# Optimization experiments

Measured on AMD Instinct MI355X. Metric: run time of the kernel, lower is better.

The kernel has to match this reference:

```python
import jax, jax.numpy as jnp
import numpy as np

B, L, IN_DIM, OUT_DIM = 8, 128, 512, 512
DEP_NUM, DEP_DIM = 45, 16


def setup_inputs() -> dict:
    key = jax.random.key(0)
    ks = jax.random.split(key, 10)
    h = jax.random.normal(ks[0], (B, L, IN_DIM), dtype=jnp.float32)
    dep_type_matrix = jax.random.randint(ks[1], (B, L, L), 0, DEP_NUM, dtype=jnp.int32)
    aspect_mask = jnp.zeros((B, L), dtype=bool).at[:, 10:14].set(True)
    # params (torch Linear convention: y = x @ W.T + b); xavier-ish scale
    def xavier(k, shape):
        fan_in, fan_out = shape[1], shape[0]
        lim = jnp.sqrt(6.0 / (fan_in + fan_out))
        return jax.random.uniform(k, shape, jnp.float32, -lim, lim)
    emb = jax.random.normal(ks[2], (DEP_NUM, DEP_DIM), dtype=jnp.float32)
    W1 = xavier(ks[3], (OUT_DIM, IN_DIM + DEP_DIM))
    b1 = jnp.zeros((OUT_DIM,), jnp.float32)
    W2 = xavier(ks[4], (OUT_DIM, IN_DIM + DEP_DIM))
    b2 = jnp.zeros((OUT_DIM,), jnp.float32)
    Wg = xavier(ks[5], (OUT_DIM, IN_DIM))
    bg = jnp.zeros((OUT_DIM,), jnp.float32)
    bias = jnp.zeros((OUT_DIM,), jnp.float32)
    return {"h": h, "dep_type_matrix": dep_type_matrix, "aspect_mask": aspect_mask,
            "emb": emb, "W1": W1, "b1": b1, "W2": W2, "b2": b2,
            "Wg": Wg, "bg": bg, "bias": bias}


def _position_aware(h, aspect_mask):
    # h: [B,L,D], aspect_mask: [B,L] bool
    Lh = h.shape[1]
    m = aspect_mask.astype(jnp.int32)
    start = jnp.argmax(m, axis=1)                       # first True
    end = Lh - 1 - jnp.argmax(jnp.flip(m, axis=1), axis=1)  # last True
    pos = jnp.arange(Lh)[None, :]                        # [1,L]
    s = start[:, None]
    e = end[:, None]
    inv_L = 1.0 / Lh
    left_w = 1.0 - (s - pos).astype(h.dtype) * inv_L
    right_w = 1.0 - (pos - e).astype(h.dtype) * inv_L
    w = jnp.where(pos < s, left_w, jnp.where(pos > e, right_w, 0.0))
    w = jnp.where(aspect_mask, 0.0, w)                   # zero on aspect words
    return h * w[:, :, None]


def reference(h, dep_type_matrix, aspect_mask, emb, W1, b1, W2, b2, Wg, bg, bias):
    D = h.shape[-1]
    h = _position_aware(h, aspect_mask)
    dep_emb = emb[dep_type_matrix]                       # [B,L,L,E]
    # split concat-linear: W(concat[h_i, e_ij]) = h_i @ Wh.T + e_ij @ Wd.T + b
    W1h, W1d = W1[:, :D], W1[:, D:]
    W2h, W2d = W2[:, :D], W2[:, D:]
    hp_i = jnp.einsum('bid,od->bio', h, W1h)[:, :, None, :] \
        + jnp.einsum('bije,oe->bijo', dep_emb, W1d) + b1   # [B,L,L,O]
    hp_j = jnp.einsum('bid,od->bio', h, W2h)[:, :, None, :] \
        + jnp.einsum('bije,oe->bijo', dep_emb, W2d) + b2   # [B,L,L,O]
    scores = jnp.exp(jnp.sum(hp_i * hp_j, axis=-1))        # [B,L,L]
    adj = (dep_type_matrix != 0).astype(scores.dtype)
    masked = scores * adj
    A = masked / (jnp.sum(masked, axis=-1, keepdims=True) + 1e-6)
    h_trans = jnp.einsum('bid,od->bio', h, Wg) + bg        # [B,L,O]
    out = jnp.einsum('bij,bjo->bio', A, h_trans) + bias
    return jax.nn.relu(out)
```

## Files before the change

kernel.cpp:

```cpp
#include <hip/hip_runtime.h>
#include <hip/hip_bf16.h>
#include <math.h>

#define NBATCH 8
#define NL 128
#define IND 512
#define DEPN 45
#define DEPD 16
#define WCOLS 528
#define NP 1664
#define C_P1 0
#define C_P2 512
#define C_HT 1024
#define C_D1 1536
#define C_D2 1581
#define C_PAD 1626

typedef __attribute__((ext_vector_type(8))) short bf16x8;
typedef __attribute__((ext_vector_type(4))) float f32x4;

__device__ inline ushort f2bf(float x) {
    __hip_bfloat16 b = __float2bfloat16(x);
    return *reinterpret_cast<ushort*>(&b);
}
__device__ inline float bf2f(ushort u) {
    __hip_bfloat16 b;
    *reinterpret_cast<ushort*>(&b) = u;
    return __bfloat162float(b);
}

__device__ __forceinline__ void gl16(const ushort* g, ushort* l) {
    __builtin_amdgcn_global_load_lds(
        (const __attribute__((address_space(1))) unsigned int*)g,
        (__attribute__((address_space(3))) unsigned int*)l, 16, 0, 0);
}

__global__ __launch_bounds__(256) void k_prep(
    const float* __restrict__ h, const unsigned char* __restrict__ mask,
    const float* __restrict__ emb,
    const float* __restrict__ W1, const float* __restrict__ W2,
    const float* __restrict__ Wg,
    const float* __restrict__ b1, const float* __restrict__ b2,
    const float* __restrict__ bg,
    ushort* __restrict__ A_hi, ushort* __restrict__ A_lo,
    ushort* __restrict__ B_hi, ushort* __restrict__ B_lo,
    float* __restrict__ bias_ext) {
    int bid = blockIdx.x;
    int tid = threadIdx.x;

    if (bid < 64) {
        int rb = bid * 16;
        int b = rb >> 7;
        __shared__ int sflag, smin, smax;
        __shared__ float w16[16];
        if (tid == 0) { sflag = 0; smin = NL; smax = -1; }
        __syncthreads();
        const int* mi = (const int*)mask;
        if (tid < 128) {
            int v0 = mi[tid], v1 = mi[tid + 128];
            if ((unsigned)v0 > 1u || (unsigned)v1 > 1u) atomicOr(&sflag, 1);
        }
        __syncthreads();
        if (tid < 128) {
            int mval = sflag ? (int)mask[b * NL + tid] : mi[b * NL + tid];
            if (mval) { atomicMin(&smin, tid); atomicMax(&smax, tid); }
        }
        __syncthreads();
        if (tid < 16) {
            int any = (smax >= 0);
            int s = any ? smin : 0;
            int e = any ? smax : (NL - 1);
            int i = (rb & 127) + tid;
            const float invL = 1.0f / (float)NL;
            float w;
            if (i < s)      w = 1.0f - (float)(s - i) * invL;
            else if (i > e) w = 1.0f - (float)(i - e) * invL;
            else            w = 0.0f;
            int mval = sflag ? (int)mask[b * NL + i] : mi[b * NL + i];
            if (mval) w = 0.0f;
            w16[tid] = w;
        }
        __syncthreads();
        for (int idx = tid; idx < 16 * 128; idx += 256) {
            int r = idx >> 7, dc = (idx & 127) << 2;
            float4 hv = *(const float4*)&h[(size_t)(rb + r) * IND + dc];
            float wv = w16[r];
            hv.x *= wv; hv.y *= wv; hv.z *= wv; hv.w *= wv;
            ushort4 hi4, lo4;
            hi4.x = f2bf(hv.x); hi4.y = f2bf(hv.y); hi4.z = f2bf(hv.z); hi4.w = f2bf(hv.w);
            lo4.x = f2bf(hv.x - bf2f(hi4.x));
            lo4.y = f2bf(hv.y - bf2f(hi4.y));
            lo4.z = f2bf(hv.z - bf2f(hi4.z));
            lo4.w = f2bf(hv.w - bf2f(hi4.w));
            *(ushort4*)&A_hi[(size_t)(rb + r) * IND + dc] = hi4;
            *(ushort4*)&A_lo[(size_t)(rb + r) * IND + dc] = lo4;
        }
        if (bid == 0) {
            for (int i = tid; i < 512; i += 256) {
                bias_ext[C_P1 + i] = b1[i];
                bias_ext[C_P2 + i] = b2[i];
                bias_ext[C_HT + i] = bg[i];
            }
            if (tid < NP - C_PAD) bias_ext[C_PAD + tid] = 0.f;
        }
    } else if (bid < 160) {
        int nb = (bid - 64) * 16;
        for (int idx = tid; idx < 16 * 128; idx += 256) {
            int r = idx >> 7, dc = (idx & 127) << 2;
            int n = nb + r;
            const float* src;
            if (n < 512)       src = W1 + (size_t)n * WCOLS + dc;
            else if (n < 1024) src = W2 + (size_t)(n - 512) * WCOLS + dc;
            else               src = Wg + (size_t)(n - 1024) * IND + dc;
            float4 wv = *(const float4*)src;
            ushort4 hi4;
            hi4.x = f2bf(wv.x); hi4.y = f2bf(wv.y); hi4.z = f2bf(wv.z); hi4.w = f2bf(wv.w);
            *(ushort4*)&B_hi[(size_t)n * IND + dc] = hi4;
            if (n >= 1024) {
                ushort4 lo4;
                lo4.x = f2bf(wv.x - bf2f(hi4.x));
                lo4.y = f2bf(wv.y - bf2f(hi4.y));
                lo4.z = f2bf(wv.z - bf2f(hi4.z));
                lo4.w = f2bf(wv.w - bf2f(hi4.w));
                *(ushort4*)&B_lo[(size_t)n * IND + dc] = lo4;
            }
        }
    } else if (bid < 162) {
        int nb = 1626 + (bid - 160) * 19;
        ushort4 z4 = {0, 0, 0, 0};
        for (int idx = tid; idx < 19 * 128; idx += 256) {
            int r = idx >> 7, dc = (idx & 127) << 2;
            *(ushort4*)&B_hi[(size_t)(nb + r) * IND + dc] = z4;
            *(ushort4*)&B_lo[(size_t)(nb + r) * IND + dc] = z4;
        }
    } else if (bid < 234) {
        int zi = bid - 162;
        int m = zi / 36;
        int rest = zi % 36;
        int dq = rest / 9;
        int tq = rest % 9;
        int tb = tq * 5;
        __shared__ float es5[5][DEPD];
        __shared__ float ys5[5][512];
        __shared__ float part[5][256];
        if (tid < 5 * DEPD) es5[tid >> 4][tid & 15] = emb[(tb + (tid >> 4)) * DEPD + (tid & 15)];
        __syncthreads();
        const float* Wdep = (m == 0) ? W2 : W1;
        for (int idx = tid; idx < 5 * 512; idx += 256) {
            int tt = idx >> 9, o = idx & 511;
            float s = 0.f;
#pragma unroll
            for (int e = 0; e < DEPD; e++) s += es5[tt][e] * Wdep[o * WCOLS + IND + e];
            ys5[tt][o] = s;
        }
        __syncthreads();
        int dloc = tid & 127, half = tid >> 7;
        const float* Wsrc = (m == 0) ? W1 : W2;
        int d = dq * 128 + dloc;
        int obase = half * 256;
        float ac0 = 0.f, ac1 = 0.f, ac2 = 0.f, ac3 = 0.f, ac4 = 0.f;
#pragma unroll 8
        for (int oo = 0; oo < 256; oo++) {
            float w = Wsrc[(size_t)(obase + oo) * WCOLS + d];
            int o = obase + oo;
            ac0 += w * ys5[0][o];
            ac1 += w * ys5[1][o];
            ac2 += w * ys5[2][o];
            ac3 += w * ys5[3][o];
            ac4 += w * ys5[4][o];
        }
        part[0][tid] = ac0; part[1][tid] = ac1; part[2][tid] = ac2;
        part[3][tid] = ac3; part[4][tid] = ac4;
        __syncthreads();
        if (half == 0) {
#pragma unroll
            for (int tt = 0; tt < 5; tt++) {
                float tot = part[tt][dloc] + part[tt][128 + dloc];
                int row = ((m == 0) ? C_D1 : C_D2) + tb + tt;
                ushort hi = f2bf(tot);
                B_hi[(size_t)row * IND + d] = hi;
                B_lo[(size_t)row * IND + d] = f2bf(tot - bf2f(hi));
            }
        }
    } else {
        int zi2 = bid - 234;
        int t = zi2 % 45;
        int m = zi2 / 45;
        __shared__ float es[DEPD];
        __shared__ float ys[512];
        __shared__ float y1s[512];
        if (tid < DEPD) es[tid] = emb[t * DEPD + tid];
        __syncthreads();
        const float* Wdep = (m == 0) ? W2 : W1;
        for (int o = tid; o < 512; o += 256) {
            float s = 0.f;
#pragma unroll
            for (int e = 0; e < DEPD; e++) s += es[e] * Wdep[o * WCOLS + IND + e];
            ys[o] = s;
        }
        if (m == 0) {
            for (int o = tid; o < 512; o += 256) {
                float s = 0.f;
#pragma unroll
                for (int e = 0; e < DEPD; e++) s += es[e] * W1[o * WCOLS + IND + e];
                y1s[o] = s;
            }
        }
        __syncthreads();
        if (tid < 64) {
            const float* bb = (m == 0) ? b1 : b2;
            float sb = 0.f;
#pragma unroll
            for (int k = 0; k < 8; k++) sb += bb[tid + k * 64] * ys[tid + k * 64];
            if (m == 0) {
#pragma unroll
                for (int k = 0; k < 8; k++) sb += y1s[tid + k * 64] * ys[tid + k * 64];
            }
            for (int off = 32; off; off >>= 1) sb += __shfl_down(sb, off, 64);
            if (tid == 0) bias_ext[((m == 0) ? C_D1 : C_D2) + t] = sb;
        }
    }
}

__global__ __launch_bounds__(256) void k3_gemm(
    const ushort* __restrict__ A_hi, const ushort* __restrict__ A_lo,
    const ushort* __restrict__ B_hi, const ushort* __restrict__ B_lo,
    const float* __restrict__ bias_ext, float* __restrict__ Pout,
    ushort* __restrict__ HTb) {
    int tid = threadIdx.x;
    int wid = tid >> 6, lane = tid & 63;
    int lrow = lane & 15;
    int mbase = blockIdx.x * 64;
    int nbase = blockIdx.y * 64;
    int mh = (wid >> 1) << 5;
    int nh = (wid & 1) << 5;

    __shared__ ushort Ah[2][8 * 64 * 8];
    __shared__ ushort Al[2][8 * 64 * 8];
    __shared__ ushort Bh[2][8 * 64 * 8];
    __shared__ ushort Bl[2][8 * 64 * 8];

    const ushort* aH = A_hi + (size_t)(mbase + lane) * IND;
    const ushort* aL = A_lo + (size_t)(mbase + lane) * IND;
    const ushort* bH = B_hi + (size_t)(nbase + lane) * IND;
    const ushort* bL = B_lo + (size_t)(nbase + lane) * IND;

    f32x4 acc00 = {0.f, 0.f, 0.f, 0.f};
    f32x4 acc01 = acc00, acc10 = acc00, acc11 = acc00;

    if (nbase >= C_HT) {
#define STAGE(BUF, C) { \
    int ck = (C) << 6; \
    if (wid == 0) { \
        _Pragma("unroll") \
        for (int g = 0; g < 8; g++) gl16(aH + ck + (g << 3), &Ah[BUF][g << 9]); \
    } else if (wid == 1) { \
        _Pragma("unroll") \
        for (int g = 0; g < 8; g++) gl16(aL + ck + (g << 3), &Al[BUF][g << 9]); \
    } else if (wid == 2) { \
        _Pragma("unroll") \
        for (int g = 0; g < 8; g++) gl16(bH + ck + (g << 3), &Bh[BUF][g << 9]); \
    } else { \
        _Pragma("unroll") \
        for (int g = 0; g < 8; g++) gl16(bL + ck + (g << 3), &Bl[BUF][g << 9]); \
    } }
        STAGE(0, 0)
        for (int c = 0; c < 8; c++) {
            int cb = c & 1;
            __syncthreads();
            if (c < 7) STAGE(cb ^ 1, c + 1)
#pragma unroll
            for (int KS = 0; KS < 2; KS++) {
                int gA = (KS << 2) + (lane >> 4);
                int ga = ((gA << 6) + mh + lrow) << 3;
                int gb = ((gA << 6) + nh + lrow) << 3;
                bf16x8 a0h = *(const bf16x8*)&Ah[cb][ga];
                bf16x8 a0l = *(const bf16x8*)&Al[cb][ga];
                bf16x8 a1h = *(const bf16x8*)&Ah[cb][ga + 128];
                bf16x8 a1l = *(const bf16x8*)&Al[cb][ga + 128];
                bf16x8 b0h = *(const bf16x8*)&Bh[cb][gb];
                bf16x8 b0l = *(const bf16x8*)&Bl[cb][gb];
                bf16x8 b1h = *(const bf16x8*)&Bh[cb][gb + 128];
                bf16x8 b1l = *(const bf16x8*)&Bl[cb][gb + 128];
                acc00 = __builtin_amdgcn_mfma_f32_16x16x32_bf16(a0h, b0h, acc00, 0, 0, 0);
                acc00 = __builtin_amdgcn_mfma_f32_16x16x32_bf16(a0h, b0l, acc00, 0, 0, 0);
                acc00 = __builtin_amdgcn_mfma_f32_16x16x32_bf16(a0l, b0h, acc00, 0, 0, 0);
                acc01 = __builtin_amdgcn_mfma_f32_16x16x32_bf16(a0h, b1h, acc01, 0, 0, 0);
                acc01 = __builtin_amdgcn_mfma_f32_16x16x32_bf16(a0h, b1l, acc01, 0, 0, 0);
                acc01 = __builtin_amdgcn_mfma_f32_16x16x32_bf16(a0l, b1h, acc01, 0, 0, 0);
                acc10 = __builtin_amdgcn_mfma_f32_16x16x32_bf16(a1h, b0h, acc10, 0, 0, 0);
                acc10 = __builtin_amdgcn_mfma_f32_16x16x32_bf16(a1h, b0l, acc10, 0, 0, 0);
                acc10 = __builtin_amdgcn_mfma_f32_16x16x32_bf16(a1l, b0h, acc10, 0, 0, 0);
                acc11 = __builtin_amdgcn_mfma_f32_16x16x32_bf16(a1h, b1h, acc11, 0, 0, 0);
                acc11 = __builtin_amdgcn_mfma_f32_16x16x32_bf16(a1h, b1l, acc11, 0, 0, 0);
                acc11 = __builtin_amdgcn_mfma_f32_16x16x32_bf16(a1l, b1h, acc11, 0, 0, 0);
            }
        }
#undef STAGE
    } else {
#define STAGEL(BUF, C) { \
    int ck = (C) << 6; \
    if (wid == 0) { \
        _Pragma("unroll") \
        for (int g = 0; g < 4; g++) gl16(aH + ck + (g << 3), &Ah[BUF][g << 9]); \
    } else if (wid == 1) { \
        _Pragma("unroll") \
        for (int g = 4; g < 8; g++) gl16(aH + ck + (g << 3), &Ah[BUF][g << 9]); \
    } else if (wid == 2) { \
        _Pragma("unroll") \
        for (int g = 0; g < 4; g++) gl16(bH + ck + (g << 3), &Bh[BUF][g << 9]); \
    } else { \
        _Pragma("unroll") \
        for (int g = 4; g < 8; g++) gl16(bH + ck + (g << 3), &Bh[BUF][g << 9]); \
    } }
        STAGEL(0, 0)
        for (int c = 0; c < 8; c++) {
            int cb = c & 1;
            __syncthreads();
            if (c < 7) STAGEL(cb ^ 1, c + 1)
#pragma unroll
            for (int KS = 0; KS < 2; KS++) {
                int gA = (KS << 2) + (lane >> 4);
                int ga = ((gA << 6) + mh + lrow) << 3;
                int gb = ((gA << 6) + nh + lrow) << 3;
                bf16x8 a0h = *(const bf16x8*)&Ah[cb][ga];
                bf16x8 a1h = *(const bf16x8*)&Ah[cb][ga + 128];
                bf16x8 b0h = *(const bf16x8*)&Bh[cb][gb];
                bf16x8 b1h = *(const bf16x8*)&Bh[cb][gb + 128];
                acc00 = __builtin_amdgcn_mfma_f32_16x16x32_bf16(a0h, b0h, acc00, 0, 0, 0);
                acc01 = __builtin_amdgcn_mfma_f32_16x16x32_bf16(a0h, b1h, acc01, 0, 0, 0);
                acc10 = __builtin_amdgcn_mfma_f32_16x16x32_bf16(a1h, b0h, acc10, 0, 0, 0);
                acc11 = __builtin_amdgcn_mfma_f32_16x16x32_bf16(a1h, b1h, acc11, 0, 0, 0);
            }
        }
#undef STAGEL
    }

    int r0 = (lane >> 4) << 2;
    int colb = nbase + nh;
    int col0 = colb + lrow;
    int col1 = col0 + 16;
    float bv0 = bias_ext[col0];
    float bv1 = bias_ext[col1];
    int rowb = mbase + mh;

    if (colb >= C_HT && colb < C_HT + 512) {
        int o0 = col0 - C_HT, o1 = col1 - C_HT;
#pragma unroll
        for (int r = 0; r < 4; ++r) {
            int row0 = rowb + r0 + r;
            int row1 = row0 + 16;
            HTb[(size_t)row0 * 512 + o0] = f2bf(acc00[r] + bv0);
            HTb[(size_t)row0 * 512 + o1] = f2bf(acc01[r] + bv1);
            HTb[(size_t)row1 * 512 + o0] = f2bf(acc10[r] + bv0);
            HTb[(size_t)row1 * 512 + o1] = f2bf(acc11[r] + bv1);
        }
    } else {
#pragma unroll
        for (int r = 0; r < 4; ++r) {
            int row0 = rowb + r0 + r;
            int row1 = row0 + 16;
            Pout[(size_t)row0 * NP + col0] = acc00[r] + bv0;
            Pout[(size_t)row0 * NP + col1] = acc01[r] + bv1;
            Pout[(size_t)row1 * NP + col0] = acc10[r] + bv0;
            Pout[(size_t)row1 * NP + col1] = acc11[r] + bv1;
        }
    }
}

__global__ __launch_bounds__(256) void k5_out(
    const float* __restrict__ P, const int* __restrict__ dep,
    const ushort* __restrict__ HTb, const float* __restrict__ bias,
    float* __restrict__ out) {
    int blk = blockIdx.x;
    int b = blk >> 5;
    int i0 = b * 128 + (blk & 31) * 4;
    int tid = threadIdx.x;
    int wr = tid >> 6, lane = tid & 63;
    __shared__ float a[4][NL];
    __shared__ float c0s[4];
    __shared__ float comb[4][48];
    __shared__ float invs[4];

    {
        const float* p1 = P + (size_t)(i0 + wr) * NP + C_P1 + lane * 8;
        const float* p2 = P + (size_t)(i0 + wr) * NP + C_P2 + lane * 8;
        float4 x0 = *(const float4*)(p1);
        float4 x1 = *(const float4*)(p1 + 4);
        float4 y0 = *(const float4*)(p2);
        float4 y1 = *(const float4*)(p2 + 4);
        float s = x0.x * y0.x + x0.y * y0.y + x0.z * y0.z + x0.w * y0.w
                + x1.x * y1.x + x1.y * y1.y + x1.z * y1.z + x1.w * y1.w;
        for (int off = 32; off; off >>= 1) s += __shfl_down(s, off, 64);
        if (lane == 0) c0s[wr] = s;
    }
    for (int idx = tid; idx < 4 * 45; idx += 256) {
        int r = idx / 45, t = idx - r * 45;
        const float* Prow = P + (size_t)(i0 + r) * NP;
        comb[r][t] = Prow[C_D1 + t] + Prow[C_D2 + t];
    }
    __syncthreads();

#pragma unroll
    for (int k = 0; k < 2; k++) {
        int idx = tid + k * 256;
        int r = idx >> 7, j = idx & 127;
        int tt = dep[(size_t)(i0 + r) * NL + j];
        a[r][j] = (tt != 0) ? expf(c0s[r] + comb[r][tt]) : 0.f;
    }
    __syncthreads();
    {
        float v = a[wr][lane] + a[wr][lane + 64];
        for (int off = 32; off; off >>= 1) v += __shfl_down(v, off, 64);
        if (lane == 0) invs[wr] = 1.0f / (v + 1e-6f);
    }
    __syncthreads();

    int o2 = tid * 2;
    float s00 = 0.f, s01 = 0.f, s10 = 0.f, s11 = 0.f;
    float s20 = 0.f, s21 = 0.f, s30 = 0.f, s31 = 0.f;
    const ushort* hp = HTb + (size_t)b * NL * 512 + o2;
#pragma unroll 8
    for (int j = 0; j < NL; j++) {
        ushort2 hv = *(const ushort2*)(hp + (size_t)j * 512);
        float h0 = bf2f(hv.x), h1 = bf2f(hv.y);
        float a0 = a[0][j], a1 = a[1][j], a2 = a[2][j], a3 = a[3][j];
        s00 += a0 * h0; s01 += a0 * h1;
        s10 += a1 * h0; s11 += a1 * h1;
        s20 += a2 * h0; s21 += a2 * h1;
        s30 += a3 * h0; s31 += a3 * h1;
    }
    float bv0 = bias[o2], bv1 = bias[o2 + 1];
    float i0v = invs[0], i1v = invs[1], i2v = invs[2], i3v = invs[3];
    float2 o;
    o.x = fmaxf(s00 * i0v + bv0, 0.f); o.y = fmaxf(s01 * i0v + bv1, 0.f);
    *(float2*)&out[(size_t)(i0 + 0) * 512 + o2] = o;
    o.x = fmaxf(s10 * i1v + bv0, 0.f); o.y = fmaxf(s11 * i1v + bv1, 0.f);
    *(float2*)&out[(size_t)(i0 + 1) * 512 + o2] = o;
    o.x = fmaxf(s20 * i2v + bv0, 0.f); o.y = fmaxf(s21 * i2v + bv1, 0.f);
    *(float2*)&out[(size_t)(i0 + 2) * 512 + o2] = o;
    o.x = fmaxf(s30 * i3v + bv0, 0.f); o.y = fmaxf(s31 * i3v + bv1, 0.f);
    *(float2*)&out[(size_t)(i0 + 3) * 512 + o2] = o;
}

extern "C" void kernel_launch(void* const* d_in, const int* in_sizes, int n_in,
                              void* d_out, int out_size, void* d_ws, size_t ws_size,
                              hipStream_t stream) {
    const float* h    = (const float*)d_in[0];
    const int* dep    = (const int*)d_in[1];
    const unsigned char* mask = (const unsigned char*)d_in[2];
    const float* emb  = (const float*)d_in[3];
    const float* W1   = (const float*)d_in[4];
    const float* b1   = (const float*)d_in[5];
    const float* W2   = (const float*)d_in[6];
    const float* b2   = (const float*)d_in[7];
    const float* Wg   = (const float*)d_in[8];
    const float* bg   = (const float*)d_in[9];
    const float* bias = (const float*)d_in[10];
    float* out = (float*)d_out;

    char* p = (char*)d_ws;
    ushort* A_hi = (ushort*)p;  p += (size_t)1024 * 512 * 2;
    ushort* A_lo = (ushort*)p;  p += (size_t)1024 * 512 * 2;
    ushort* B_hi = (ushort*)p;  p += (size_t)NP * 512 * 2;
    ushort* B_lo = (ushort*)p;  p += (size_t)NP * 512 * 2;
    ushort* HTb = (ushort*)p;   p += (size_t)1024 * 512 * 2;
    float* bias_ext = (float*)p; p += NP * 4;
    float* Pout = (float*)p;

    k_prep<<<324, 256, 0, stream>>>(h, mask, emb, W1, W2, Wg, b1, b2, bg,
                                    A_hi, A_lo, B_hi, B_lo, bias_ext);
    dim3 g3(16, 26);
    k3_gemm<<<g3, 256, 0, stream>>>(A_hi, A_lo, B_hi, B_lo, bias_ext, Pout, HTb);
    k5_out<<<256, 256, 0, stream>>>(Pout, dep, HTb, bias, out);
}
```

Baseline: 48.32 us.

## Fuse P1·P2 row dot product into GEMM epilogue with atomic accumulation

The GEMM blocks for the two projection column ranges now compute both the W1h and W2h tiles together against the same A tile, so the A tile is loaded once for both. Each block forms the partial per-row dot product of the biased projections in registers, reduces it with shuffles, and atomically adds it into a new c0 buffer. This removes the full 512-column fp32 P1/P2 writes and the matching reads in the output kernel, and shrinks the grid from 26 to 18 column blocks. In exchange it adds atomics, which make the summation order nondeterministic, and it needs a zero-init of the buffer in the prep kernel.

```diff
diff --git a/kernel.cpp b/kernel.cpp
--- a/kernel.cpp
+++ b/kernel.cpp
@@ -44,7 +44,7 @@
     const float* __restrict__ bg,
     ushort* __restrict__ A_hi, ushort* __restrict__ A_lo,
     ushort* __restrict__ B_hi, ushort* __restrict__ B_lo,
-    float* __restrict__ bias_ext) {
+    float* __restrict__ bias_ext, float* __restrict__ c0buf) {
     int bid = blockIdx.x;
     int tid = threadIdx.x;
 
@@ -102,6 +102,7 @@
                 bias_ext[C_HT + i] = bg[i];
             }
             if (tid < NP - C_PAD) bias_ext[C_PAD + tid] = 0.f;
+            for (int i = tid; i < 1024; i += 256) c0buf[i] = 0.f;
         }
     } else if (bid < 160) {
         int nb = (bid - 64) * 16;
@@ -226,29 +227,30 @@
     const ushort* __restrict__ A_hi, const ushort* __restrict__ A_lo,
     const ushort* __restrict__ B_hi, const ushort* __restrict__ B_lo,
     const float* __restrict__ bias_ext, float* __restrict__ Pout,
-    ushort* __restrict__ HTb) {
+    ushort* __restrict__ HTb, float* __restrict__ c0buf) {
     int tid = threadIdx.x;
     int wid = tid >> 6, lane = tid & 63;
     int lrow = lane & 15;
     int mbase = blockIdx.x * 64;
-    int nbase = blockIdx.y * 64;
+    int y = blockIdx.y;
     int mh = (wid >> 1) << 5;
     int nh = (wid & 1) << 5;
+    int r0 = (lane >> 4) << 2;
+    int rowb = mbase + mh;
 
     __shared__ ushort Ah[2][8 * 64 * 8];
     __shared__ ushort Al[2][8 * 64 * 8];
     __shared__ ushort Bh[2][8 * 64 * 8];
     __shared__ ushort Bl[2][8 * 64 * 8];
 
-    const ushort* aH = A_hi + (size_t)(mbase + lane) * IND;
-    const ushort* aL = A_lo + (size_t)(mbase + lane) * IND;
-    const ushort* bH = B_hi + (size_t)(nbase + lane) * IND;
-    const ushort* bL = B_lo + (size_t)(nbase + lane) * IND;
-
-    f32x4 acc00 = {0.f, 0.f, 0.f, 0.f};
-    f32x4 acc01 = acc00, acc10 = acc00, acc11 = acc00;
-
-    if (nbase >= C_HT) {
+    if (y >= 8) {
+        int nbase = 1024 + ((y - 8) << 6);
+        const ushort* aH = A_hi + (size_t)(mbase + lane) * IND;
+        const ushort* aL = A_lo + (size_t)(mbase + lane) * IND;
+        const ushort* bH = B_hi + (size_t)(nbase + lane) * IND;
+        const ushort* bL = B_lo + (size_t)(nbase + lane) * IND;
+        f32x4 acc00 = {0.f, 0.f, 0.f, 0.f};
+        f32x4 acc01 = acc00, acc10 = acc00, acc11 = acc00;
 #define STAGE(BUF, C) { \
     int ck = (C) << 6; \
     if (wid == 0) { \
@@ -297,27 +299,58 @@
             }
         }
 #undef STAGE
+        int colb = nbase + nh;
+        int col0 = colb + lrow;
+        int col1 = col0 + 16;
+        float bv0 = bias_ext[col0];
+        float bv1 = bias_ext[col1];
+        if (colb < C_D1) {
+            int o0 = col0 - C_HT, o1 = col1 - C_HT;
+#pragma unroll
+            for (int r = 0; r < 4; ++r) {
+                int row0 = rowb + r0 + r;
+                int row1 = row0 + 16;
+                HTb[(size_t)row0 * 512 + o0] = f2bf(acc00[r] + bv0);
+                HTb[(size_t)row0 * 512 + o1] = f2bf(acc01[r] + bv1);
+                HTb[(size_t)row1 * 512 + o0] = f2bf(acc10[r] + bv0);
+                HTb[(size_t)row1 * 512 + o1] = f2bf(acc11[r] + bv1);
+            }
+        } else {
+#pragma unroll
+            for (int r = 0; r < 4; ++r) {
+                int row0 = rowb + r0 + r;
+                int row1 = row0 + 16;
+                Pout[(size_t)row0 * NP + col0] = acc00[r] + bv0;
+                Pout[(size_t)row0 * NP + col1] = acc01[r] + bv1;
+                Pout[(size_t)row1 * NP + col0] = acc10[r] + bv0;
+                Pout[(size_t)row1 * NP + col1] = acc11[r] + bv1;
+            }
+        }
     } else {
-#define STAGEL(BUF, C) { \
+        int j = y;
+        const ushort* aH  = A_hi + (size_t)(mbase + lane) * IND;
+        const ushort* b1H = B_hi + (size_t)((j << 6) + lane) * IND;
+        const ushort* b2H = B_hi + (size_t)(512 + (j << 6) + lane) * IND;
+        f32x4 z4 = {0.f, 0.f, 0.f, 0.f};
+        f32x4 p00 = z4, p01 = z4, p10 = z4, p11 = z4;
+        f32x4 q00 = z4, q01 = z4, q10 = z4, q11 = z4;
+#define STAGEP(BUF, C) { \
     int ck = (C) << 6; \
     if (wid == 0) { \
         _Pragma("unroll") \
-        for (int g = 0; g < 4; g++) gl16(aH + ck + (g << 3), &Ah[BUF][g << 9]); \
+        for (int g = 0; g < 8; g++) gl16(aH + ck + (g << 3), &Ah[BUF][g << 9]); \
     } else if (wid == 1) { \
         _Pragma("unroll") \
-        for (int g = 4; g < 8; g++) gl16(aH + ck + (g << 3), &Ah[BUF][g << 9]); \
+        for (int g = 0; g < 8; g++) gl16(b1H + ck + (g << 3), &Bh[BUF][g << 9]); \
     } else if (wid == 2) { \
         _Pragma("unroll") \
-        for (int g = 0; g < 4; g++) gl16(bH + ck + (g << 3), &Bh[BUF][g << 9]); \
-    } else { \
-        _Pragma("unroll") \
-        for (int g = 4; g < 8; g++) gl16(bH + ck + (g << 3), &Bh[BUF][g << 9]); \
+        for (int g = 0; g < 8; g++) gl16(b2H + ck + (g << 3), &Al[BUF][g << 9]); \
     } }
-        STAGEL(0, 0)
+        STAGEP(0, 0)
         for (int c = 0; c < 8; c++) {
             int cb = c & 1;
             __syncthreads();
-            if (c < 7) STAGEL(cb ^ 1, c + 1)
+            if (c < 7) STAGEP(cb ^ 1, c + 1)
 #pragma unroll
             for (int KS = 0; KS < 2; KS++) {
                 int gA = (KS << 2) + (lane >> 4);
@@ -325,45 +358,38 @@
                 int gb = ((gA << 6) + nh + lrow) << 3;
                 bf16x8 a0h = *(const bf16x8*)&Ah[cb][ga];
                 bf16x8 a1h = *(const bf16x8*)&Ah[cb][ga + 128];
-                bf16x8 b0h = *(const bf16x8*)&Bh[cb][gb];
-                bf16x8 b1h = *(const bf16x8*)&Bh[cb][gb + 128];
-                acc00 = __builtin_amdgcn_mfma_f32_16x16x32_bf16(a0h, b0h, acc00, 0, 0, 0);
-                acc01 = __builtin_amdgcn_mfma_f32_16x16x32_bf16(a0h, b1h, acc01, 0, 0, 0);
-                acc10 = __builtin_amdgcn_mfma_f32_16x16x32_bf16(a1h, b0h, acc10, 0, 0, 0);
-                acc11 = __builtin_amdgcn_mfma_f32_16x16x32_bf16(a1h, b1h, acc11, 0, 0, 0);
-            }
-        }
-#undef STAGEL
-    }
-
-    int r0 = (lane >> 4) << 2;
-    int colb = nbase + nh;
-    int col0 = colb + lrow;
-    int col1 = col0 + 16;
-    float bv0 = bias_ext[col0];
-    float bv1 = bias_ext[col1];
-    int rowb = mbase + mh;
-
-    if (colb >= C_HT && colb < C_HT + 512) {
-        int o0 = col0 - C_HT, o1 = col1 - C_HT;
+                bf16x8 b10 = *(const bf16x8*)&Bh[cb][gb];
+                bf16x8 b11 = *(const bf16x8*)&Bh[cb][gb + 128];
+                bf16x8 b20 = *(const bf16x8*)&Al[cb][gb];
+                bf16x8 b21 = *(const bf16x8*)&Al[cb][gb + 128];
+                p00 = __builtin_amdgcn_mfma_f32_16x16x32_bf16(a0h, b10, p00, 0, 0, 0);
+                p01 = __builtin_amdgcn_mfma_f32_16x16x32_bf16(a0h, b11, p01, 0, 0, 0);
+                p10 = __builtin_amdgcn_mfma_f32_16x16x32_bf16(a1h, b10, p10, 0, 0, 0);
+                p11 = __builtin_amdgcn_mfma_f32_16x16x32_bf16(a1h, b11, p11, 0, 0, 0);
+                q00 = __builtin_amdgcn_mfma_f32_16x16x32_bf16(a0h, b20, q00, 0, 0, 0);
+                q01 = __builtin_amdgcn_mfma_f32_16x16x32_bf16(a0h, b21, q01, 0, 0, 0);
+                q10 = __builtin_amdgcn_mfma_f32_16x16x32_bf16(a1h, b20, q10, 0, 0, 0);
+                q11 = __builtin_amdgcn_mfma_f32_16x16x32_bf16(a1h, b21, q11, 0, 0, 0);
+            }
+        }
+#undef STAGEP
+        int o0 = (j << 6) + nh + lrow;
+        float b1v0 = bias_ext[C_P1 + o0], b1v1 = bias_ext[C_P1 + o0 + 16];
+        float b2v0 = bias_ext[C_P2 + o0], b2v1 = bias_ext[C_P2 + o0 + 16];
 #pragma unroll
         for (int r = 0; r < 4; ++r) {
-            int row0 = rowb + r0 + r;
-            int row1 = row0 + 16;
-            HTb[(size_t)row0 * 512 + o0] = f2bf(acc00[r] + bv0);
-            HTb[(size_t)row0 * 512 + o1] = f2bf(acc01[r] + bv1);
-            HTb[(size_t)row1 * 512 + o0] = f2bf(acc10[r] + bv0);
-            HTb[(size_t)row1 * 512 + o1] = f2bf(acc11[r] + bv1);
-        }
-    } else {
-#pragma unroll
-        for (int r = 0; r < 4; ++r) {
-            int row0 = rowb + r0 + r;
-            int row1 = row0 + 16;
-            Pout[(size_t)row0 * NP + col0] = acc00[r] + bv0;
-            Pout[(size_t)row0 * NP + col1] = acc01[r] + bv1;
-            Pout[(size_t)row1 * NP + col0] = acc10[r] + bv0;
-            Pout[(size_t)row1 * NP + col1] = acc11[r] + bv1;
+            float sa = (p00[r] + b1v0) * (q00[r] + b2v0)
+                     + (p01[r] + b1v1) * (q01[r] + b2v1);
+            float sb = (p10[r] + b1v0) * (q10[r] + b2v0)
+                     + (p11[r] + b1v1) * (q11[r] + b2v1);
+            sa += __shfl_xor(sa, 1, 16); sa += __shfl_xor(sa, 2, 16);
+            sa += __shfl_xor(sa, 4, 16); sa += __shfl_xor(sa, 8, 16);
+            sb += __shfl_xor(sb, 1, 16); sb += __shfl_xor(sb, 2, 16);
+            sb += __shfl_xor(sb, 4, 16); sb += __shfl_xor(sb, 8, 16);
+            if (lrow == 0) {
+                atomicAdd(&c0buf[rowb + r0 + r], sa);
+                atomicAdd(&c0buf[rowb + 16 + r0 + r], sb);
+            }
         }
     }
 }
@@ -371,7 +397,7 @@
 __global__ __launch_bounds__(256) void k5_out(
     const float* __restrict__ P, const int* __restrict__ dep,
     const ushort* __restrict__ HTb, const float* __restrict__ bias,
-    float* __restrict__ out) {
+    const float* __restrict__ c0buf, float* __restrict__ out) {
     int blk = blockIdx.x;
     int b = blk >> 5;
     int i0 = b * 128 + (blk & 31) * 4;
@@ -382,18 +408,7 @@
     __shared__ float comb[4][48];
     __shared__ float invs[4];
 
-    {
-        const float* p1 = P + (size_t)(i0 + wr) * NP + C_P1 + lane * 8;
-        const float* p2 = P + (size_t)(i0 + wr) * NP + C_P2 + lane * 8;
-        float4 x0 = *(const float4*)(p1);
-        float4 x1 = *(const float4*)(p1 + 4);
-        float4 y0 = *(const float4*)(p2);
-        float4 y1 = *(const float4*)(p2 + 4);
-        float s = x0.x * y0.x + x0.y * y0.y + x0.z * y0.z + x0.w * y0.w
-                + x1.x * y1.x + x1.y * y1.y + x1.z * y1.z + x1.w * y1.w;
-        for (int off = 32; off; off >>= 1) s += __shfl_down(s, off, 64);
-        if (lane == 0) c0s[wr] = s;
-    }
+    if (tid < 4) c0s[tid] = c0buf[i0 + tid];
     for (int idx = tid; idx < 4 * 45; idx += 256) {
         int r = idx / 45, t = idx - r * 45;
         const float* Prow = P + (size_t)(i0 + r) * NP;
@@ -466,11 +481,13 @@
     ushort* B_lo = (ushort*)p;  p += (size_t)NP * 512 * 2;
     ushort* HTb = (ushort*)p;   p += (size_t)1024 * 512 * 2;
     float* bias_ext = (float*)p; p += NP * 4;
+    float* c0buf = (float*)p;   p += 1024 * 4;
     float* Pout = (float*)p;
 
     k_prep<<<324, 256, 0, stream>>>(h, mask, emb, W1, W2, Wg, b1, b2, bg,
-                                    A_hi, A_lo, B_hi, B_lo, bias_ext);
-    dim3 g3(16, 26);
-    k3_gemm<<<g3, 256, 0, stream>>>(A_hi, A_lo, B_hi, B_lo, bias_ext, Pout, HTb);
-    k5_out<<<256, 256, 0, stream>>>(Pout, dep, HTb, bias, out);
-}
+                                    A_hi, A_lo, B_hi, B_lo, bias_ext, c0buf);
+    dim3 g3(16, 18);
+    k3_gemm<<<g3, 256, 0, stream>>>(A_hi, A_lo, B_hi, B_lo, bias_ext, Pout,
+                                    HTb, c0buf);
+    k5_out<<<256, 256, 0, stream>>>(Pout, dep, HTb, bias, c0buf, out);
+}
```

After: 49.93 us. 3.3% more time.
